# Kernel optimization log

Hardware: AMD Instinct MI355X
Metric: run time of the kernel (lower is better)

## Reference

```python
import jax, jax.numpy as jnp
import numpy as np

GAMMA = 0.1


def spmm(edge_index, edge_weight, feat, n_nodes):
    # y[dst] += w * feat[src]  -- sparse adjacency @ feat via gather/scatter
    src = edge_index[0]
    dst = edge_index[1]
    msgs = feat[src] * edge_weight[:, None]  # [E, d]
    return jax.ops.segment_sum(msgs, dst, num_segments=n_nodes)


def setup_inputs() -> dict:
    key = jax.random.key(0)
    ks = jax.random.split(key, 12)
    N, F, H, O = 50000, 500, 64, 16
    E, Ek = 1600000, 1000000
    x = jax.random.normal(ks[0], (N, F), dtype=jnp.float32)
    edge_index = jax.random.randint(ks[1], (2, E), 0, N, dtype=jnp.int32)
    edge_weight = jax.random.uniform(ks[2], (E,), dtype=jnp.float32)
    knn_edge_index = jax.random.randint(ks[3], (2, Ek), 0, N, dtype=jnp.int32)
    knn_edge_weight = jax.random.uniform(ks[4], (Ek,), dtype=jnp.float32)
    # glorot-ish scaled params
    W0 = jax.random.normal(ks[5], (F, H), dtype=jnp.float32) * (1.0 / np.sqrt(F))
    W1 = jax.random.normal(ks[6], (H, O), dtype=jnp.float32) * (1.0 / np.sqrt(H))
    score0 = jax.random.normal(ks[7], (F, 1), dtype=jnp.float32) * (1.0 / np.sqrt(F))
    score1 = jax.random.normal(ks[8], (H, 1), dtype=jnp.float32) * (1.0 / np.sqrt(H))
    Dk0 = jax.random.normal(ks[9], (F, 1), dtype=jnp.float32) * (1.0 / np.sqrt(F))
    Dk1 = jax.random.normal(ks[10], (H, 1), dtype=jnp.float32) * (1.0 / np.sqrt(H))
    z = jnp.zeros((1,), dtype=jnp.float32)
    return {
        "x": x, "edge_index": edge_index, "edge_weight": edge_weight,
        "knn_edge_index": knn_edge_index, "knn_edge_weight": knn_edge_weight,
        "W0": W0, "W1": W1,
        "score0": score0, "sbias0": z, "score1": score1, "sbias1": z,
        "Dk0": Dk0, "Dbias0": z, "Dk1": Dk1, "Dbias1": z,
    }


def reference(x, edge_index, edge_weight, knn_edge_index, knn_edge_weight,
              W0, W1, score0, sbias0, score1, sbias1,
              Dk0, Dbias0, Dk1, Dbias1):
    N = x.shape[0]
    layers = [(W0, score0, sbias0, Dk0, Dbias0),
              (W1, score1, sbias1, Dk1, Dbias1)]
    for W, sc, sb, dkw, dkb in layers:
        s = jax.nn.sigmoid(x @ sc + sb)          # [N, 1] gate
        Dk = x @ dkw + dkb                        # [N, 1] degree-like scale
        xW = x @ W                                # shared linear transform
        agg = spmm(edge_index, edge_weight, xW, N)        # GCNConv(x, adj)
        agg_knn = spmm(knn_edge_index, knn_edge_weight, xW, N)  # GCNConv(x, adj_knn)
        # acts are identity (acts=[None] and final act None); dropout off (eval)
        x = s * agg + (1.0 - s) * agg_knn + GAMMA * Dk * xW
    return x
```

## Files before the change

### kernel.cpp

```cpp
#include <hip/hip_runtime.h>
#include <math.h>

#define GAMMA 0.1f

typedef float f32x4 __attribute__((ext_vector_type(4)));
typedef short short4v __attribute__((ext_vector_type(4)));
typedef short short8 __attribute__((ext_vector_type(8)));

static __device__ __forceinline__ unsigned short f2bf(float f) {
  union { float f; unsigned u; } v; v.f = f;
  unsigned r = v.u + 0x7FFF + ((v.u >> 16) & 1);
  return (unsigned short)(r >> 16);
}
static __device__ __forceinline__ float bf2f(unsigned short b) {
  union { unsigned u; float f; } v; v.u = ((unsigned)b) << 16;
  return v.f;
}

__global__ __launch_bounds__(256) void setup_fused(
    int* __restrict__ bcnt2, int ncnt,
    const float* __restrict__ W0, const float* __restrict__ sc0,
    const float* __restrict__ dk0, unsigned short* __restrict__ Bt0, int F,
    const float* __restrict__ W1, const float* __restrict__ sc1,
    const float* __restrict__ dk1, unsigned short* __restrict__ Bt1) {
  int b = blockIdx.x;
  int t = threadIdx.x;
  if (b < 2) {
    int i = b * 256 + t;
    if (i < ncnt) bcnt2[i] = 0;
  } else if (b < 162) {
    int i = (b - 2) * 256 + t;
    int c = i >> 9;
    int k = i & 511;
    float v = 0.f;
    if (k < F) {
      if (c < 64) v = W0[(size_t)k * 64 + c];
      else if (c == 64) v = sc0[k];
      else if (c == 65) v = dk0[k];
    }
    Bt0[(size_t)((k >> 3) * 80 + c) * 8 + (k & 7)] = f2bf(v);
  } else {
    int i = (b - 162) * 256 + t;
    int c = i >> 6;
    int k = i & 63;
    float v;
    if (c < 16) v = W1[(size_t)k * 16 + c];
    else if (c == 16) v = sc1[k];
    else if (c == 17) v = dk1[k];
    else v = 0.f;
    Bt1[(size_t)((k >> 3) * 32 + c) * 8 + (k & 7)] = f2bf(v);
  }
}

#define BIN_CHUNK 8192

__global__ __launch_bounds__(256) void gemm_fill_fused(
    const float* __restrict__ A, const unsigned short* __restrict__ Bt3,
    const float* __restrict__ sb, const float* __restrict__ db,
    unsigned short* __restrict__ outW, float* __restrict__ s,
    float* __restrict__ Dk, int N, int Kact, int gemmBlocks,
    const int* __restrict__ eiA, const float* __restrict__ ewA, int EA,
    int* __restrict__ gcurA, int2* __restrict__ recA,
    const int* __restrict__ eiK, const float* __restrict__ ewK, int EK,
    int* __restrict__ gcurK, int2* __restrict__ recK, int nchA) {
  constexpr int KPAD = 512;
  constexpr int KSPLIT = 4, RPB = 16;
  constexpr int KS_PER = (KPAD / 32) / KSPLIT;
  constexpr int CFRAGS = 5, OUTFRAGS = 4, COLS = 80;
  constexpr int H = OUTFRAGS * 16;
  __shared__ unsigned short Ald[RPB * KPAD];
  __shared__ float red[(KSPLIT - 1) * 64 * CFRAGS * 4];
  __shared__ int scnt[256];
  __shared__ int scur[256];

  const int t = threadIdx.x;

  if (blockIdx.x < gemmBlocks) {
    const int rowBase = blockIdx.x * RPB;

#pragma unroll
    for (int it = 0; it < (RPB * KPAD) / (256 * 4); ++it) {
      int li = it * 1024 + t * 4;
      int row = li >> 9;
      int col = li & 511;
      int grow = rowBase + row;
      f32x4 v = (f32x4)0.f;
      if (grow < N && col < Kact)
        v = *(const f32x4*)(A + (size_t)grow * Kact + col);
      short4v bb;
#pragma unroll
      for (int j = 0; j < 4; ++j) bb[j] = (short)f2bf(v[j]);
      int byte = row * (KPAD * 2) + ((col * 2) ^ ((row & 7) << 4));
      *(short4v*)((char*)Ald + byte) = bb;
    }
    __syncthreads();

    const int kslice = t >> 6;
    const int l = t & 63;
    const int kgrp = l >> 4;
    const int lc = l & 15;
    const int lrow = lc;
    const int rowD = rowBase + kgrp * 4;

    f32x4 acc[CFRAGS];
#pragma unroll
    for (int i = 0; i < CFRAGS; ++i) acc[i] = (f32x4)0.f;

    const int rbyte = lrow * (KPAD * 2);
    const int rswz = (lrow & 7) << 4;
#pragma unroll
    for (int kk = 0; kk < KS_PER; ++kk) {
      const int ks = kslice * KS_PER + kk;
      short8 av = *(const short8*)((char*)Ald +
                                   (rbyte + ((ks * 64 + kgrp * 16) ^ rswz)));
      const unsigned short* bbase =
          Bt3 + (size_t)((ks * 4 + kgrp) * COLS + lc) * 8;
#pragma unroll
      for (int fc = 0; fc < CFRAGS; ++fc) {
        short8 bv = *(const short8*)(bbase + fc * 128);
        acc[fc] =
            __builtin_amdgcn_mfma_f32_16x16x32_bf16(av, bv, acc[fc], 0, 0, 0);
      }
    }

    if (kslice > 0) {
      float* dst = red + ((kslice - 1) * 64 + l) * (CFRAGS * 4);
#pragma unroll
      for (int fc = 0; fc < CFRAGS; ++fc)
#pragma unroll
        for (int r = 0; r < 4; ++r) dst[fc * 4 + r] = acc[fc][r];
    }
    __syncthreads();
    if (kslice == 0) {
#pragma unroll
      for (int s2 = 1; s2 < KSPLIT; ++s2) {
        const float* src2 = red + ((s2 - 1) * 64 + l) * (CFRAGS * 4);
#pragma unroll
        for (int fc = 0; fc < CFRAGS; ++fc)
#pragma unroll
          for (int r = 0; r < 4; ++r) acc[fc][r] += src2[fc * 4 + r];
      }
#pragma unroll
      for (int fc = 0; fc < OUTFRAGS; ++fc) {
#pragma unroll
        for (int r = 0; r < 4; ++r) {
          int gr = rowD + r;
          if (gr < N) outW[(size_t)gr * H + fc * 16 + lc] = f2bf(acc[fc][r]);
        }
      }
      if (lc < 2) {
        f32x4 g = acc[CFRAGS - 1];
#pragma unroll
        for (int r = 0; r < 4; ++r) {
          int gr = rowD + r;
          if (gr < N) {
            if (lc == 0) s[gr] = 1.f / (1.f + expf(-(g[r] + sb[0])));
            else Dk[gr] = g[r] + db[0];
          }
        }
      }
    }
  } else {
    int fb = blockIdx.x - gemmBlocks;
    const int* ei;
    const float* ew;
    int E, chunk;
    int* gcur;
    int2* rec;
    if (fb < nchA) {
      ei = eiA; ew = ewA; E = EA; gcur = gcurA; rec = recA; chunk = fb;
    } else {
      ei = eiK; ew = ewK; E = EK; gcur = gcurK; rec = recK;
      chunk = fb - nchA;
    }
    scnt[t] = 0;
    __syncthreads();
    const int base = chunk * BIN_CHUNK;
    for (int k = t; k < BIN_CHUNK; k += 256) {
      int e = base + k;
      if (e < E) atomicAdd(&scnt[ei[E + e] >> 8], 1);
    }
    __syncthreads();
    if (scnt[t]) scur[t] = atomicAdd(&gcur[t], scnt[t]);
    __syncthreads();
    for (int k = t; k < BIN_CHUNK; k += 256) {
      int e = base + k;
      if (e < E) {
        int src = ei[e];
        int dst = ei[E + e];
        int pos = atomicAdd(&scur[dst >> 8], 1);
        rec[pos] = make_int2(((dst & 255) << 16) | src, __float_as_int(ew[e]));
      }
    }
  }
}

__global__ __launch_bounds__(512) void bucket_count2(
    const int* __restrict__ eiA, int EA, int* __restrict__ bcntA,
    const int* __restrict__ eiK, int EK, int* __restrict__ bcntK, int nchA) {
  const int* ei;
  int E, chunk;
  int* bcnt;
  if (blockIdx.x < nchA) { ei = eiA; E = EA; bcnt = bcntA; chunk = blockIdx.x; }
  else { ei = eiK; E = EK; bcnt = bcntK; chunk = blockIdx.x - nchA; }
  __shared__ int lc[256];
  if (threadIdx.x < 256) lc[threadIdx.x] = 0;
  __syncthreads();
  const int base = chunk * BIN_CHUNK;
  for (int k = threadIdx.x; k < BIN_CHUNK; k += 512) {
    int e = base + k;
    if (e < E) atomicAdd(&lc[ei[E + e] >> 8], 1);
  }
  __syncthreads();
  if (threadIdx.x < 256 && lc[threadIdx.x])
    atomicAdd(&bcnt[threadIdx.x], lc[threadIdx.x]);
}

__global__ __launch_bounds__(512) void bucket_scan2(
    int* __restrict__ bcntA, int* __restrict__ boffA, int* __restrict__ gcurA,
    int* __restrict__ bcntK, int* __restrict__ boffK, int* __restrict__ gcurK,
    int nb) {
  int* bcnt = blockIdx.x ? bcntK : bcntA;
  int* boff = blockIdx.x ? boffK : boffA;
  int* gcur = blockIdx.x ? gcurK : gcurA;
  __shared__ int sh[512];
  int t = threadIdx.x;
  int v = (t < nb) ? bcnt[t] : 0;
  sh[t] = v;
  __syncthreads();
  int acc = v;
  for (int off = 1; off < 512; off <<= 1) {
    int xx = (t >= off) ? sh[t - off] : 0;
    __syncthreads();
    acc += xx;
    sh[t] = acc;
    __syncthreads();
  }
  if (t < nb) {
    boff[t] = acc - v;
    gcur[t] = acc - v;
  }
  if (t == nb - 1) boff[nb] = acc;
}

__global__ __launch_bounds__(512) void tile_sort2(
    const int2* __restrict__ recRawA, const int* __restrict__ boffA,
    unsigned* __restrict__ recSA, int* __restrict__ rpA,
    const int2* __restrict__ recRawK, const int* __restrict__ boffK,
    unsigned* __restrict__ recSK, int* __restrict__ rpK, int N, int nb) {
  const int2* recRaw;
  const int* boff;
  unsigned* recS;
  int* rp;
  int tile;
  if (blockIdx.x < nb) {
    recRaw = recRawA; boff = boffA; recS = recSA; rp = rpA; tile = blockIdx.x;
  } else {
    recRaw = recRawK; boff = boffK; recS = recSK; rp = rpK;
    tile = blockIdx.x - nb;
  }
  __shared__ int cnt[256];
  __shared__ int sc[256];
  __shared__ int cur[256];
  const int lo = boff[tile], hi = boff[tile + 1];
  const int t = threadIdx.x;
  if (t < 256) cnt[t] = 0;
  __syncthreads();
  for (int j = lo + t; j < hi; j += 512)
    atomicAdd(&cnt[recRaw[j].x >> 16], 1);
  __syncthreads();
  if (t < 256) sc[t] = cnt[t];
  __syncthreads();
  for (int off = 1; off < 256; off <<= 1) {
    int v = 0;
    if (t < 256 && t >= off) v = sc[t - off];
    __syncthreads();
    if (t < 256) sc[t] += v;
    __syncthreads();
  }
  if (t < 256) {
    int excl = sc[t] - cnt[t];
    cur[t] = excl;
    int n = tile * 256 + t;
    if (n < N) rp[n] = lo + excl;
  }
  if (tile == nb - 1 && t == 0) rp[N] = hi;
  __syncthreads();
  for (int j = lo + t; j < hi; j += 512) {
    int2 r = recRaw[j];
    int pos = lo + atomicAdd(&cur[r.x >> 16], 1);
    recS[pos] = ((unsigned)f2bf(__int_as_float(r.y)) << 16) |
                (unsigned)(r.x & 0xFFFF);
  }
}

template <int KPAD, int CFRAGS, int OUTFRAGS, int COLS>
__global__ __launch_bounds__(256) void mfma_linear_bf(
    const unsigned short* __restrict__ Aptr, const unsigned short* __restrict__ Bt3,
    const float* __restrict__ sb, const float* __restrict__ db,
    unsigned short* __restrict__ outW, float* __restrict__ s,
    float* __restrict__ Dk, int N, int Kact) {
  constexpr int H = OUTFRAGS * 16;
  constexpr int KSPLIT = 2, RG = 2, RPB = 32;
  constexpr int KS_PER = (KPAD / 32) / KSPLIT;
  __shared__ float red[(KSPLIT - 1) * RG * 64 * CFRAGS * 4];

  const int w = threadIdx.x >> 6;
  const int rowgrp = w % RG;
  const int kslice = w / RG;
  const int l = threadIdx.x & 63;
  const int kgrp = l >> 4;
  const int lc = l & 15;
  const int rowA = blockIdx.x * RPB + rowgrp * 16 + lc;
  const int rowD = blockIdx.x * RPB + rowgrp * 16 + kgrp * 4;
  const int rowSafe = (rowA < N) ? rowA : 0;

  f32x4 acc[CFRAGS];
#pragma unroll
  for (int i = 0; i < CFRAGS; ++i) acc[i] = (f32x4)0.f;

#pragma unroll
  for (int kk = 0; kk < KS_PER; ++kk) {
    const int ks = kslice * KS_PER + kk;
    const int kb = ks * 32 + kgrp * 8;
    short8 av = *(const short8*)(Aptr + (size_t)rowSafe * Kact + kb);
    const unsigned short* bbase =
        Bt3 + (size_t)((ks * 4 + kgrp) * COLS + lc) * 8;
#pragma unroll
    for (int fc = 0; fc < CFRAGS; ++fc) {
      short8 bv = *(const short8*)(bbase + fc * 128);
      acc[fc] = __builtin_amdgcn_mfma_f32_16x16x32_bf16(av, bv, acc[fc], 0, 0, 0);
    }
  }

  if (kslice > 0) {
    float* dst = red + ((rowgrp)*64 + l) * (CFRAGS * 4);
#pragma unroll
    for (int fc = 0; fc < CFRAGS; ++fc)
#pragma unroll
      for (int r = 0; r < 4; ++r) dst[fc * 4 + r] = acc[fc][r];
  }
  __syncthreads();
  if (kslice == 0) {
    const float* src2 = red + ((rowgrp)*64 + l) * (CFRAGS * 4);
#pragma unroll
    for (int fc = 0; fc < CFRAGS; ++fc)
#pragma unroll
      for (int r = 0; r < 4; ++r) acc[fc][r] += src2[fc * 4 + r];

#pragma unroll
    for (int fc = 0; fc < OUTFRAGS; ++fc) {
#pragma unroll
      for (int r = 0; r < 4; ++r) {
        int gr = rowD + r;
        if (gr < N) outW[(size_t)gr * H + fc * 16 + lc] = f2bf(acc[fc][r]);
      }
    }
    if (lc < 2) {
      f32x4 g = acc[CFRAGS - 1];
#pragma unroll
      for (int r = 0; r < 4; ++r) {
        int gr = rowD + r;
        if (gr < N) {
          if (lc == 0) s[gr] = 1.f / (1.f + expf(-(g[r] + sb[0])));
          else Dk[gr] = g[r] + db[0];
        }
      }
    }
  }
}

static __device__ __forceinline__ float gather64(
    const int* __restrict__ rp, const unsigned* __restrict__ rec,
    const unsigned short* __restrict__ feat, int n, int h) {
  int b = rp[n], e = rp[n + 1];
  float a[16];
#pragma unroll
  for (int u = 0; u < 16; ++u) a[u] = 0.f;
  int j = b;
  for (; j + 16 <= e; j += 16) {
#pragma unroll
    for (int u = 0; u < 16; ++u) {
      unsigned r = rec[j + u];
      a[u] += bf2f((unsigned short)(r >> 16)) *
              bf2f(feat[(size_t)(r & 0xFFFF) * 64 + h]);
    }
  }
  for (; j + 4 <= e; j += 4) {
#pragma unroll
    for (int u = 0; u < 4; ++u) {
      unsigned r = rec[j + u];
      a[u] += bf2f((unsigned short)(r >> 16)) *
              bf2f(feat[(size_t)(r & 0xFFFF) * 64 + h]);
    }
  }
  for (; j < e; ++j) {
    unsigned r = rec[j];
    a[0] += bf2f((unsigned short)(r >> 16)) *
            bf2f(feat[(size_t)(r & 0xFFFF) * 64 + h]);
  }
  float t0 = ((a[0] + a[1]) + (a[2] + a[3])) + ((a[4] + a[5]) + (a[6] + a[7]));
  float t1 = ((a[8] + a[9]) + (a[10] + a[11])) +
             ((a[12] + a[13]) + (a[14] + a[15]));
  return t0 + t1;
}

__global__ __launch_bounds__(256) void agg_combine64(
    const int* __restrict__ rpA, const unsigned* __restrict__ recA,
    const int* __restrict__ rpK, const unsigned* __restrict__ recK,
    const unsigned short* __restrict__ feat, const float* __restrict__ s,
    const float* __restrict__ Dk, unsigned short* __restrict__ outp, int N) {
  int n = __builtin_amdgcn_readfirstlane((blockIdx.x * 256 + threadIdx.x) >> 6);
  if (n >= N) return;
  int h = threadIdx.x & 63;
  float aA = gather64(rpA, recA, feat, n, h);
  float aK = gather64(rpK, recK, feat, n, h);
  float sv = s[n];
  float res = sv * aA + (1.f - sv) * aK +
              GAMMA * Dk[n] * bf2f(feat[(size_t)n * 64 + h]);
  outp[(size_t)n * 64 + h] = f2bf(res);
}

static __device__ __forceinline__ float gather16(
    const int* __restrict__ rp, const unsigned* __restrict__ rec,
    const unsigned short* __restrict__ feat, int n, int h) {
  int b = rp[n], e = rp[n + 1];
  float a0 = 0.f, a1 = 0.f, a2 = 0.f, a3 = 0.f;
  float a4 = 0.f, a5 = 0.f, a6 = 0.f, a7 = 0.f;
  int j = b;
  for (; j + 8 <= e; j += 8) {
    unsigned q0 = rec[j + 0];
    unsigned q1 = rec[j + 1];
    unsigned q2 = rec[j + 2];
    unsigned q3 = rec[j + 3];
    unsigned q4 = rec[j + 4];
    unsigned q5 = rec[j + 5];
    unsigned q6 = rec[j + 6];
    unsigned q7 = rec[j + 7];
    a0 += bf2f((unsigned short)(q0 >> 16)) *
          bf2f(feat[(size_t)(q0 & 0xFFFF) * 16 + h]);
    a1 += bf2f((unsigned short)(q1 >> 16)) *
          bf2f(feat[(size_t)(q1 & 0xFFFF) * 16 + h]);
    a2 += bf2f((unsigned short)(q2 >> 16)) *
          bf2f(feat[(size_t)(q2 & 0xFFFF) * 16 + h]);
    a3 += bf2f((unsigned short)(q3 >> 16)) *
          bf2f(feat[(size_t)(q3 & 0xFFFF) * 16 + h]);
    a4 += bf2f((unsigned short)(q4 >> 16)) *
          bf2f(feat[(size_t)(q4 & 0xFFFF) * 16 + h]);
    a5 += bf2f((unsigned short)(q5 >> 16)) *
          bf2f(feat[(size_t)(q5 & 0xFFFF) * 16 + h]);
    a6 += bf2f((unsigned short)(q6 >> 16)) *
          bf2f(feat[(size_t)(q6 & 0xFFFF) * 16 + h]);
    a7 += bf2f((unsigned short)(q7 >> 16)) *
          bf2f(feat[(size_t)(q7 & 0xFFFF) * 16 + h]);
  }
  for (; j < e; ++j) {
    unsigned q = rec[j];
    a0 += bf2f((unsigned short)(q >> 16)) *
          bf2f(feat[(size_t)(q & 0xFFFF) * 16 + h]);
  }
  return ((a0 + a1) + (a2 + a3)) + ((a4 + a5) + (a6 + a7));
}

__global__ __launch_bounds__(256) void agg_combine16(
    const int* __restrict__ rpA, const unsigned* __restrict__ recA,
    const int* __restrict__ rpK, const unsigned* __restrict__ recK,
    const unsigned short* __restrict__ feat, const float* __restrict__ s,
    const float* __restrict__ Dk, float* __restrict__ outp, int N) {
  int tid = blockIdx.x * 256 + threadIdx.x;
  int n = tid >> 4;
  int h = tid & 15;
  if (n >= N) return;
  float aA = gather16(rpA, recA, feat, n, h);
  float aK = gather16(rpK, recK, feat, n, h);
  float sv = s[n];
  float res = sv * aA + (1.f - sv) * aK +
              GAMMA * Dk[n] * bf2f(feat[(size_t)n * 16 + h]);
  outp[(size_t)n * 16 + h] = res;
}

extern "C" void kernel_launch(void* const* d_in, const int* in_sizes, int n_in,
                              void* d_out, int out_size, void* d_ws, size_t ws_size,
                              hipStream_t stream) {
  const float* x = (const float*)d_in[0];
  const int* edge_index = (const int*)d_in[1];
  const float* edge_weight = (const float*)d_in[2];
  const int* knn_edge_index = (const int*)d_in[3];
  const float* knn_edge_weight = (const float*)d_in[4];
  const float* W0 = (const float*)d_in[5];
  const float* W1 = (const float*)d_in[6];
  const float* score0 = (const float*)d_in[7];
  const float* sbias0 = (const float*)d_in[8];
  const float* score1 = (const float*)d_in[9];
  const float* sbias1 = (const float*)d_in[10];
  const float* Dk0 = (const float*)d_in[11];
  const float* Dbias0 = (const float*)d_in[12];
  const float* Dk1 = (const float*)d_in[13];
  const float* Dbias1 = (const float*)d_in[14];

  const int F = in_sizes[7];
  const int N = in_sizes[0] / F;
  const int E = in_sizes[2];
  const int Ek = in_sizes[4];
  (void)n_in; (void)ws_size; (void)out_size;

  const int nb = (N + 255) / 256;

  char* cur = (char*)d_ws;
  auto alloc = [&](size_t bytes) {
    char* p = cur;
    cur += (bytes + 255) & ~(size_t)255;
    return (void*)p;
  };
  float* sbuf = (float*)alloc((size_t)N * 4);
  float* dkbuf = (float*)alloc((size_t)N * 4);
  int* bcnt2 = (int*)alloc((size_t)2 * nb * 4);
  int* bcntA = bcnt2;
  int* bcntK = bcnt2 + nb;
  int* boffA = (int*)alloc((size_t)(nb + 1) * 4);
  int* boffK = (int*)alloc((size_t)(nb + 1) * 4);
  int* gcurA = (int*)alloc((size_t)nb * 4);
  int* gcurK = (int*)alloc((size_t)nb * 4);
  int* rpA = (int*)alloc((size_t)(N + 1) * 4);
  int* rpK = (int*)alloc((size_t)(N + 1) * 4);
  unsigned* recA = (unsigned*)alloc((size_t)E * 4);
  unsigned* recK = (unsigned*)alloc((size_t)Ek * 4);
  unsigned short* Bt0 = (unsigned short*)alloc((size_t)80 * 512 * 2);
  unsigned short* Bt1 = (unsigned short*)alloc((size_t)32 * 64 * 2);
  int2* recRawA = (int2*)alloc((size_t)E * 8);
  int2* recRawK = (int2*)alloc((size_t)Ek * 8);
  unsigned short* xWb = (unsigned short*)alloc((size_t)N * 64 * 2);
  unsigned short* x1b = (unsigned short*)alloc((size_t)N * 64 * 2);
  unsigned short* xW1b = (unsigned short*)alloc((size_t)N * 16 * 2);

  const int nchA = (E + BIN_CHUNK - 1) / BIN_CHUNK;
  const int nchK = (Ek + BIN_CHUNK - 1) / BIN_CHUNK;
  const int gemmBlocksL0 = (N + 15) / 16;
  const int gemmBlocksL1 = (N + 31) / 32;
  const int agg64Blocks = (int)(((size_t)N * 64 + 255) / 256);
  const int agg16Blocks = (int)(((size_t)N * 16 + 255) / 256);

  setup_fused<<<170, 256, 0, stream>>>(bcnt2, 2 * nb, W0, score0, Dk0, Bt0, F,
                                       W1, score1, Dk1, Bt1);
  bucket_count2<<<nchA + nchK, 512, 0, stream>>>(edge_index, E, bcntA,
                                                 knn_edge_index, Ek, bcntK,
                                                 nchA);
  bucket_scan2<<<2, 512, 0, stream>>>(bcntA, boffA, gcurA, bcntK, boffK,
                                      gcurK, nb);
  gemm_fill_fused<<<gemmBlocksL0 + nchA + nchK, 256, 0, stream>>>(
      x, Bt0, sbias0, Dbias0, xWb, sbuf, dkbuf, N, F, gemmBlocksL0,
      edge_index, edge_weight, E, gcurA, recRawA, knn_edge_index,
      knn_edge_weight, Ek, gcurK, recRawK, nchA);
  tile_sort2<<<2 * nb, 512, 0, stream>>>(recRawA, boffA, recA, rpA, recRawK,
                                         boffK, recK, rpK, N, nb);
  agg_combine64<<<agg64Blocks, 256, 0, stream>>>(rpA, recA, rpK, recK, xWb,
                                                 sbuf, dkbuf, x1b, N);
  mfma_linear_bf<64, 2, 1, 32><<<gemmBlocksL1, 256, 0, stream>>>(
      x1b, Bt1, sbias1, Dbias1, xW1b, sbuf, dkbuf, N, 64);
  agg_combine16<<<agg16Blocks, 256, 0, stream>>>(rpA, recA, rpK, recK, xW1b,
                                                 sbuf, dkbuf, (float*)d_out, N);
}
```

Measured before the change: 181.6 us.

## Unfuse layer-0 GEMM from binning, reuse per-chunk counts, alias raw records with features

```diff
diff --git a/kernel.cpp b/kernel.cpp
--- a/kernel.cpp
+++ b/kernel.cpp
@@ -52,152 +52,187 @@
   }
 }
 
-#define BIN_CHUNK 8192
-
-__global__ __launch_bounds__(256) void gemm_fill_fused(
+template <int CFRAGS, int OUTFRAGS, int COLS>
+__global__ __launch_bounds__(256) void mfma_linear_l0(
     const float* __restrict__ A, const unsigned short* __restrict__ Bt3,
     const float* __restrict__ sb, const float* __restrict__ db,
     unsigned short* __restrict__ outW, float* __restrict__ s,
-    float* __restrict__ Dk, int N, int Kact, int gemmBlocks,
-    const int* __restrict__ eiA, const float* __restrict__ ewA, int EA,
-    int* __restrict__ gcurA, int2* __restrict__ recA,
-    const int* __restrict__ eiK, const float* __restrict__ ewK, int EK,
-    int* __restrict__ gcurK, int2* __restrict__ recK, int nchA) {
+    float* __restrict__ Dk, int N, int Kact) {
   constexpr int KPAD = 512;
   constexpr int KSPLIT = 4, RPB = 16;
   constexpr int KS_PER = (KPAD / 32) / KSPLIT;
-  constexpr int CFRAGS = 5, OUTFRAGS = 4, COLS = 80;
   constexpr int H = OUTFRAGS * 16;
   __shared__ unsigned short Ald[RPB * KPAD];
   __shared__ float red[(KSPLIT - 1) * 64 * CFRAGS * 4];
-  __shared__ int scnt[256];
-  __shared__ int scur[256];
 
   const int t = threadIdx.x;
-
-  if (blockIdx.x < gemmBlocks) {
-    const int rowBase = blockIdx.x * RPB;
-
-#pragma unroll
-    for (int it = 0; it < (RPB * KPAD) / (256 * 4); ++it) {
-      int li = it * 1024 + t * 4;
-      int row = li >> 9;
-      int col = li & 511;
-      int grow = rowBase + row;
-      f32x4 v = (f32x4)0.f;
-      if (grow < N && col < Kact)
-        v = *(const f32x4*)(A + (size_t)grow * Kact + col);
-      short4v bb;
-#pragma unroll
-      for (int j = 0; j < 4; ++j) bb[j] = (short)f2bf(v[j]);
-      int byte = row * (KPAD * 2) + ((col * 2) ^ ((row & 7) << 4));
-      *(short4v*)((char*)Ald + byte) = bb;
-    }
-    __syncthreads();
-
-    const int kslice = t >> 6;
-    const int l = t & 63;
-    const int kgrp = l >> 4;
-    const int lc = l & 15;
-    const int lrow = lc;
-    const int rowD = rowBase + kgrp * 4;
-
-    f32x4 acc[CFRAGS];
-#pragma unroll
-    for (int i = 0; i < CFRAGS; ++i) acc[i] = (f32x4)0.f;
-
-    const int rbyte = lrow * (KPAD * 2);
-    const int rswz = (lrow & 7) << 4;
-#pragma unroll
-    for (int kk = 0; kk < KS_PER; ++kk) {
-      const int ks = kslice * KS_PER + kk;
-      short8 av = *(const short8*)((char*)Ald +
-                                   (rbyte + ((ks * 64 + kgrp * 16) ^ rswz)));
-      const unsigned short* bbase =
-          Bt3 + (size_t)((ks * 4 + kgrp) * COLS + lc) * 8;
-#pragma unroll
-      for (int fc = 0; fc < CFRAGS; ++fc) {
-        short8 bv = *(const short8*)(bbase + fc * 128);
-        acc[fc] =
-            __builtin_amdgcn_mfma_f32_16x16x32_bf16(av, bv, acc[fc], 0, 0, 0);
+  const int rowBase = blockIdx.x * RPB;
+
+#pragma unroll
+  for (int it = 0; it < (RPB * KPAD) / (256 * 4); ++it) {
+    int li = it * 1024 + t * 4;
+    int row = li >> 9;
+    int col = li & 511;
+    int grow = rowBase + row;
+    f32x4 v = (f32x4)0.f;
+    if (grow < N && col < Kact)
+      v = *(const f32x4*)(A + (size_t)grow * Kact + col);
+    short4v b;
+#pragma unroll
+    for (int j = 0; j < 4; ++j) b[j] = (short)f2bf(v[j]);
+    int byte = row * (KPAD * 2) + ((col * 2) ^ ((row & 7) << 4));
+    *(short4v*)((char*)Ald + byte) = b;
+  }
+  __syncthreads();
+
+  const int kslice = t >> 6;
+  const int l = t & 63;
+  const int kgrp = l >> 4;
+  const int lc = l & 15;
+  const int lrow = lc;
+  const int rowD = rowBase + kgrp * 4;
+
+  f32x4 acc[CFRAGS];
+#pragma unroll
+  for (int i = 0; i < CFRAGS; ++i) acc[i] = (f32x4)0.f;
+
+  const int rbyte = lrow * (KPAD * 2);
+  const int rswz = (lrow & 7) << 4;
+#pragma unroll
+  for (int kk = 0; kk < KS_PER; ++kk) {
+    const int ks = kslice * KS_PER + kk;
+    short8 av = *(const short8*)((char*)Ald +
+                                 (rbyte + ((ks * 64 + kgrp * 16) ^ rswz)));
+    const unsigned short* bbase =
+        Bt3 + (size_t)((ks * 4 + kgrp) * COLS + lc) * 8;
+#pragma unroll
+    for (int fc = 0; fc < CFRAGS; ++fc) {
+      short8 bv = *(const short8*)(bbase + fc * 128);
+      acc[fc] = __builtin_amdgcn_mfma_f32_16x16x32_bf16(av, bv, acc[fc], 0, 0, 0);
+    }
+  }
+
+  if (kslice > 0) {
+    float* dst = red + ((kslice - 1) * 64 + l) * (CFRAGS * 4);
+#pragma unroll
+    for (int fc = 0; fc < CFRAGS; ++fc)
+#pragma unroll
+      for (int r = 0; r < 4; ++r) dst[fc * 4 + r] = acc[fc][r];
+  }
+  __syncthreads();
+  if (kslice == 0) {
+#pragma unroll
+    for (int s2 = 1; s2 < KSPLIT; ++s2) {
+      const float* src2 = red + ((s2 - 1) * 64 + l) * (CFRAGS * 4);
+#pragma unroll
+      for (int fc = 0; fc < CFRAGS; ++fc)
+#pragma unroll
+        for (int r = 0; r < 4; ++r) acc[fc][r] += src2[fc * 4 + r];
+    }
+#pragma unroll
+    for (int fc = 0; fc < OUTFRAGS; ++fc) {
+#pragma unroll
+      for (int r = 0; r < 4; ++r) {
+        int gr = rowD + r;
+        if (gr < N) outW[(size_t)gr * H + fc * 16 + lc] = f2bf(acc[fc][r]);
       }
     }
-
-    if (kslice > 0) {
-      float* dst = red + ((kslice - 1) * 64 + l) * (CFRAGS * 4);
-#pragma unroll
-      for (int fc = 0; fc < CFRAGS; ++fc)
-#pragma unroll
-        for (int r = 0; r < 4; ++r) dst[fc * 4 + r] = acc[fc][r];
-    }
-    __syncthreads();
-    if (kslice == 0) {
-#pragma unroll
-      for (int s2 = 1; s2 < KSPLIT; ++s2) {
-        const float* src2 = red + ((s2 - 1) * 64 + l) * (CFRAGS * 4);
-#pragma unroll
-        for (int fc = 0; fc < CFRAGS; ++fc)
-#pragma unroll
-          for (int r = 0; r < 4; ++r) acc[fc][r] += src2[fc * 4 + r];
-      }
-#pragma unroll
-      for (int fc = 0; fc < OUTFRAGS; ++fc) {
-#pragma unroll
-        for (int r = 0; r < 4; ++r) {
-          int gr = rowD + r;
-          if (gr < N) outW[(size_t)gr * H + fc * 16 + lc] = f2bf(acc[fc][r]);
+    if (lc < 2) {
+      f32x4 g = acc[CFRAGS - 1];
+#pragma unroll
+      for (int r = 0; r < 4; ++r) {
+        int gr = rowD + r;
+        if (gr < N) {
+          if (lc == 0) s[gr] = 1.f / (1.f + expf(-(g[r] + sb[0])));
+          else Dk[gr] = g[r] + db[0];
         }
       }
-      if (lc < 2) {
-        f32x4 g = acc[CFRAGS - 1];
-#pragma unroll
-        for (int r = 0; r < 4; ++r) {
-          int gr = rowD + r;
-          if (gr < N) {
-            if (lc == 0) s[gr] = 1.f / (1.f + expf(-(g[r] + sb[0])));
-            else Dk[gr] = g[r] + db[0];
-          }
+    }
+  }
+}
+
+template <int KPAD, int CFRAGS, int OUTFRAGS, int COLS>
+__global__ __launch_bounds__(256) void mfma_linear_bf(
+    const unsigned short* __restrict__ Aptr, const unsigned short* __restrict__ Bt3,
+    const float* __restrict__ sb, const float* __restrict__ db,
+    unsigned short* __restrict__ outW, float* __restrict__ s,
+    float* __restrict__ Dk, int N, int Kact) {
+  constexpr int H = OUTFRAGS * 16;
+  constexpr int KSPLIT = 2, RG = 2, RPB = 32;
+  constexpr int KS_PER = (KPAD / 32) / KSPLIT;
+  __shared__ float red[(KSPLIT - 1) * RG * 64 * CFRAGS * 4];
+
+  const int w = threadIdx.x >> 6;
+  const int rowgrp = w % RG;
+  const int kslice = w / RG;
+  const int l = threadIdx.x & 63;
+  const int kgrp = l >> 4;
+  const int lc = l & 15;
+  const int rowA = blockIdx.x * RPB + rowgrp * 16 + lc;
+  const int rowD = blockIdx.x * RPB + rowgrp * 16 + kgrp * 4;
+  const int rowSafe = (rowA < N) ? rowA : 0;
+
+  f32x4 acc[CFRAGS];
+#pragma unroll
+  for (int i = 0; i < CFRAGS; ++i) acc[i] = (f32x4)0.f;
+
+#pragma unroll
+  for (int kk = 0; kk < KS_PER; ++kk) {
+    const int ks = kslice * KS_PER + kk;
+    const int kb = ks * 32 + kgrp * 8;
+    short8 av = *(const short8*)(Aptr + (size_t)rowSafe * Kact + kb);
+    const unsigned short* bbase =
+        Bt3 + (size_t)((ks * 4 + kgrp) * COLS + lc) * 8;
+#pragma unroll
+    for (int fc = 0; fc < CFRAGS; ++fc) {
+      short8 bv = *(const short8*)(bbase + fc * 128);
+      acc[fc] = __builtin_amdgcn_mfma_f32_16x16x32_bf16(av, bv, acc[fc], 0, 0, 0);
+    }
+  }
+
+  if (kslice > 0) {
+    float* dst = red + ((rowgrp)*64 + l) * (CFRAGS * 4);
+#pragma unroll
+    for (int fc = 0; fc < CFRAGS; ++fc)
+#pragma unroll
+      for (int r = 0; r < 4; ++r) dst[fc * 4 + r] = acc[fc][r];
+  }
+  __syncthreads();
+  if (kslice == 0) {
+    const float* src2 = red + ((rowgrp)*64 + l) * (CFRAGS * 4);
+#pragma unroll
+    for (int fc = 0; fc < CFRAGS; ++fc)
+#pragma unroll
+      for (int r = 0; r < 4; ++r) acc[fc][r] += src2[fc * 4 + r];
+
+#pragma unroll
+    for (int fc = 0; fc < OUTFRAGS; ++fc) {
+#pragma unroll
+      for (int r = 0; r < 4; ++r) {
+        int gr = rowD + r;
+        if (gr < N) outW[(size_t)gr * H + fc * 16 + lc] = f2bf(acc[fc][r]);
+      }
+    }
+    if (lc < 2) {
+      f32x4 g = acc[CFRAGS - 1];
+#pragma unroll
+      for (int r = 0; r < 4; ++r) {
+        int gr = rowD + r;
+        if (gr < N) {
+          if (lc == 0) s[gr] = 1.f / (1.f + expf(-(g[r] + sb[0])));
+          else Dk[gr] = g[r] + db[0];
         }
       }
     }
-  } else {
-    int fb = blockIdx.x - gemmBlocks;
-    const int* ei;
-    const float* ew;
-    int E, chunk;
-    int* gcur;
-    int2* rec;
-    if (fb < nchA) {
-      ei = eiA; ew = ewA; E = EA; gcur = gcurA; rec = recA; chunk = fb;
-    } else {
-      ei = eiK; ew = ewK; E = EK; gcur = gcurK; rec = recK;
-      chunk = fb - nchA;
-    }
-    scnt[t] = 0;
-    __syncthreads();
-    const int base = chunk * BIN_CHUNK;
-    for (int k = t; k < BIN_CHUNK; k += 256) {
-      int e = base + k;
-      if (e < E) atomicAdd(&scnt[ei[E + e] >> 8], 1);
-    }
-    __syncthreads();
-    if (scnt[t]) scur[t] = atomicAdd(&gcur[t], scnt[t]);
-    __syncthreads();
-    for (int k = t; k < BIN_CHUNK; k += 256) {
-      int e = base + k;
-      if (e < E) {
-        int src = ei[e];
-        int dst = ei[E + e];
-        int pos = atomicAdd(&scur[dst >> 8], 1);
-        rec[pos] = make_int2(((dst & 255) << 16) | src, __float_as_int(ew[e]));
-      }
-    }
-  }
-}
+  }
+}
+
+#define BIN_CHUNK 8192
 
 __global__ __launch_bounds__(512) void bucket_count2(
     const int* __restrict__ eiA, int EA, int* __restrict__ bcntA,
-    const int* __restrict__ eiK, int EK, int* __restrict__ bcntK, int nchA) {
+    const int* __restrict__ eiK, int EK, int* __restrict__ bcntK, int nchA,
+    int* __restrict__ pcnt) {
   const int* ei;
   int E, chunk;
   int* bcnt;
@@ -212,8 +247,11 @@
     if (e < E) atomicAdd(&lc[ei[E + e] >> 8], 1);
   }
   __syncthreads();
-  if (threadIdx.x < 256 && lc[threadIdx.x])
-    atomicAdd(&bcnt[threadIdx.x], lc[threadIdx.x]);
+  if (threadIdx.x < 256) {
+    int c = lc[threadIdx.x];
+    pcnt[blockIdx.x * 256 + threadIdx.x] = c;
+    if (c) atomicAdd(&bcnt[threadIdx.x], c);
+  }
 }
 
 __global__ __launch_bounds__(512) void bucket_scan2(
@@ -241,6 +279,41 @@
     gcur[t] = acc - v;
   }
   if (t == nb - 1) boff[nb] = acc;
+}
+
+__global__ __launch_bounds__(512) void bin_fill2(
+    const int* __restrict__ eiA, const float* __restrict__ ewA, int EA,
+    int* __restrict__ gcurA, int2* __restrict__ recA,
+    const int* __restrict__ eiK, const float* __restrict__ ewK, int EK,
+    int* __restrict__ gcurK, int2* __restrict__ recK, int nchA,
+    const int* __restrict__ pcnt) {
+  const int* ei;
+  const float* ew;
+  int E, chunk;
+  int* gcur;
+  int2* rec;
+  if (blockIdx.x < nchA) {
+    ei = eiA; ew = ewA; E = EA; gcur = gcurA; rec = recA; chunk = blockIdx.x;
+  } else {
+    ei = eiK; ew = ewK; E = EK; gcur = gcurK; rec = recK;
+    chunk = blockIdx.x - nchA;
+  }
+  __shared__ int scur[256];
+  if (threadIdx.x < 256) {
+    int c = pcnt[blockIdx.x * 256 + threadIdx.x];
+    scur[threadIdx.x] = c ? atomicAdd(&gcur[threadIdx.x], c) : 0;
+  }
+  __syncthreads();
+  const int base = chunk * BIN_CHUNK;
+  for (int k = threadIdx.x; k < BIN_CHUNK; k += 512) {
+    int e = base + k;
+    if (e < E) {
+      int src = ei[e];
+      int dst = ei[E + e];
+      int pos = atomicAdd(&scur[dst >> 8], 1);
+      rec[pos] = make_int2(((dst & 255) << 16) | src, __float_as_int(ew[e]));
+    }
+  }
 }
 
 __global__ __launch_bounds__(512) void tile_sort2(
@@ -291,82 +364,6 @@
     int pos = lo + atomicAdd(&cur[r.x >> 16], 1);
     recS[pos] = ((unsigned)f2bf(__int_as_float(r.y)) << 16) |
                 (unsigned)(r.x & 0xFFFF);
-  }
-}
-
-template <int KPAD, int CFRAGS, int OUTFRAGS, int COLS>
-__global__ __launch_bounds__(256) void mfma_linear_bf(
-    const unsigned short* __restrict__ Aptr, const unsigned short* __restrict__ Bt3,
-    const float* __restrict__ sb, const float* __restrict__ db,
-    unsigned short* __restrict__ outW, float* __restrict__ s,
-    float* __restrict__ Dk, int N, int Kact) {
-  constexpr int H = OUTFRAGS * 16;
-  constexpr int KSPLIT = 2, RG = 2, RPB = 32;
-  constexpr int KS_PER = (KPAD / 32) / KSPLIT;
-  __shared__ float red[(KSPLIT - 1) * RG * 64 * CFRAGS * 4];
-
-  const int w = threadIdx.x >> 6;
-  const int rowgrp = w % RG;
-  const int kslice = w / RG;
-  const int l = threadIdx.x & 63;
-  const int kgrp = l >> 4;
-  const int lc = l & 15;
-  const int rowA = blockIdx.x * RPB + rowgrp * 16 + lc;
-  const int rowD = blockIdx.x * RPB + rowgrp * 16 + kgrp * 4;
-  const int rowSafe = (rowA < N) ? rowA : 0;
-
-  f32x4 acc[CFRAGS];
-#pragma unroll
-  for (int i = 0; i < CFRAGS; ++i) acc[i] = (f32x4)0.f;
-
-#pragma unroll
-  for (int kk = 0; kk < KS_PER; ++kk) {
-    const int ks = kslice * KS_PER + kk;
-    const int kb = ks * 32 + kgrp * 8;
-    short8 av = *(const short8*)(Aptr + (size_t)rowSafe * Kact + kb);
-    const unsigned short* bbase =
-        Bt3 + (size_t)((ks * 4 + kgrp) * COLS + lc) * 8;
-#pragma unroll
-    for (int fc = 0; fc < CFRAGS; ++fc) {
-      short8 bv = *(const short8*)(bbase + fc * 128);
-      acc[fc] = __builtin_amdgcn_mfma_f32_16x16x32_bf16(av, bv, acc[fc], 0, 0, 0);
-    }
-  }
-
-  if (kslice > 0) {
-    float* dst = red + ((rowgrp)*64 + l) * (CFRAGS * 4);
-#pragma unroll
-    for (int fc = 0; fc < CFRAGS; ++fc)
-#pragma unroll
-      for (int r = 0; r < 4; ++r) dst[fc * 4 + r] = acc[fc][r];
-  }
-  __syncthreads();
-  if (kslice == 0) {
-    const float* src2 = red + ((rowgrp)*64 + l) * (CFRAGS * 4);
-#pragma unroll
-    for (int fc = 0; fc < CFRAGS; ++fc)
-#pragma unroll
-      for (int r = 0; r < 4; ++r) acc[fc][r] += src2[fc * 4 + r];
-
-#pragma unroll
-    for (int fc = 0; fc < OUTFRAGS; ++fc) {
-#pragma unroll
-      for (int r = 0; r < 4; ++r) {
-        int gr = rowD + r;
-        if (gr < N) outW[(size_t)gr * H + fc * 16 + lc] = f2bf(acc[fc][r]);
-      }
-    }
-    if (lc < 2) {
-      f32x4 g = acc[CFRAGS - 1];
-#pragma unroll
-      for (int r = 0; r < 4; ++r) {
-        int gr = rowD + r;
-        if (gr < N) {
-          if (lc == 0) s[gr] = 1.f / (1.f + expf(-(g[r] + sb[0])));
-          else Dk[gr] = g[r] + db[0];
-        }
-      }
-    }
   }
 }
 
@@ -505,6 +502,8 @@
   (void)n_in; (void)ws_size; (void)out_size;
 
   const int nb = (N + 255) / 256;
+  const int nchA = (E + BIN_CHUNK - 1) / BIN_CHUNK;
+  const int nchK = (Ek + BIN_CHUNK - 1) / BIN_CHUNK;
 
   char* cur = (char*)d_ws;
   auto alloc = [&](size_t bytes) {
@@ -523,18 +522,18 @@
   int* gcurK = (int*)alloc((size_t)nb * 4);
   int* rpA = (int*)alloc((size_t)(N + 1) * 4);
   int* rpK = (int*)alloc((size_t)(N + 1) * 4);
+  int* pcnt = (int*)alloc((size_t)(nchA + nchK) * 256 * 4);
   unsigned* recA = (unsigned*)alloc((size_t)E * 4);
   unsigned* recK = (unsigned*)alloc((size_t)Ek * 4);
   unsigned short* Bt0 = (unsigned short*)alloc((size_t)80 * 512 * 2);
   unsigned short* Bt1 = (unsigned short*)alloc((size_t)32 * 64 * 2);
-  int2* recRawA = (int2*)alloc((size_t)E * 8);
-  int2* recRawK = (int2*)alloc((size_t)Ek * 8);
-  unsigned short* xWb = (unsigned short*)alloc((size_t)N * 64 * 2);
-  unsigned short* x1b = (unsigned short*)alloc((size_t)N * 64 * 2);
-  unsigned short* xW1b = (unsigned short*)alloc((size_t)N * 16 * 2);
-
-  const int nchA = (E + BIN_CHUNK - 1) / BIN_CHUNK;
-  const int nchK = (Ek + BIN_CHUNK - 1) / BIN_CHUNK;
+  char* uni = (char*)alloc((size_t)(E + Ek) * 8);
+  int2* recRawA = (int2*)uni;
+  int2* recRawK = recRawA + E;
+  unsigned short* xWb = (unsigned short*)uni;
+  unsigned short* x1b = xWb + (size_t)N * 64;
+  unsigned short* xW1b = x1b + (size_t)N * 64;
+
   const int gemmBlocksL0 = (N + 15) / 16;
   const int gemmBlocksL1 = (N + 31) / 32;
   const int agg64Blocks = (int)(((size_t)N * 64 + 255) / 256);
@@ -544,15 +543,17 @@
                                        W1, score1, Dk1, Bt1);
   bucket_count2<<<nchA + nchK, 512, 0, stream>>>(edge_index, E, bcntA,
                                                  knn_edge_index, Ek, bcntK,
-                                                 nchA);
+                                                 nchA, pcnt);
   bucket_scan2<<<2, 512, 0, stream>>>(bcntA, boffA, gcurA, bcntK, boffK,
                                       gcurK, nb);
-  gemm_fill_fused<<<gemmBlocksL0 + nchA + nchK, 256, 0, stream>>>(
-      x, Bt0, sbias0, Dbias0, xWb, sbuf, dkbuf, N, F, gemmBlocksL0,
-      edge_index, edge_weight, E, gcurA, recRawA, knn_edge_index,
-      knn_edge_weight, Ek, gcurK, recRawK, nchA);
+  bin_fill2<<<nchA + nchK, 512, 0, stream>>>(edge_index, edge_weight, E,
+                                             gcurA, recRawA, knn_edge_index,
+                                             knn_edge_weight, Ek, gcurK,
+                                             recRawK, nchA, pcnt);
   tile_sort2<<<2 * nb, 512, 0, stream>>>(recRawA, boffA, recA, rpA, recRawK,
                                          boffK, recK, rpK, N, nb);
+  mfma_linear_l0<5, 4, 80><<<gemmBlocksL0, 256, 0, stream>>>(
+      x, Bt0, sbias0, Dbias0, xWb, sbuf, dkbuf, N, F);
   agg_combine64<<<agg64Blocks, 256, 0, stream>>>(rpA, recA, rpK, recK, xWb,
                                                  sbuf, dkbuf, x1b, N);
   mfma_linear_bf<64, 2, 1, 32><<<gemmBlocksL1, 256, 0, stream>>>(
```

New measurement: 169.0 us, median of 3. 1.07x faster.
